# Optimization experiments

Measured on AMD Instinct MI355X. Metric: run time of the kernel, lower is better.

Reference implementation:

```python
import jax, jax.numpy as jnp
import numpy as np

N = 50000
E = 800000
IN_CH = 128
OUT_CH = 32
HEADS = 10
NEG_SLOPE = 0.2
NUM_GRAPHS = 512


def gat_layer(x, W, a_src, a_dst, b, src, dst, heads, out_ch):
    n = x.shape[0]
    h = (x @ W).reshape(n, heads, out_ch)            # [N,H,C]
    e_src = jnp.einsum('nhc,hc->nh', h, a_src)       # [N,H]
    e_dst = jnp.einsum('nhc,hc->nh', h, a_dst)       # [N,H]
    alpha = jax.nn.leaky_relu(e_src[src] + e_dst[dst], negative_slope=NEG_SLOPE)  # [E,H]
    amax = jax.ops.segment_max(alpha, dst, num_segments=n)
    amax = jnp.where(jnp.isneginf(amax), 0.0, amax)
    ex = jnp.exp(alpha - amax[dst])                   # [E,H]
    denom = jax.ops.segment_sum(ex, dst, num_segments=n)
    coef = ex / (denom[dst] + 1e-16)                  # segment softmax over incoming edges
    msg = h[src] * coef[:, :, None]                   # [E,H,C]
    out = jax.ops.segment_sum(msg, dst, num_segments=n)
    return out.reshape(n, heads * out_ch) + b


def setup_inputs() -> dict:
    key = jax.random.key(0)
    ks = jax.random.split(key, 12)
    x = jax.random.normal(ks[0], (N, IN_CH), dtype=jnp.float32)
    edge_index = jax.random.randint(ks[1], (2, E), 0, N, dtype=jnp.int32)
    batch = jnp.sort(jax.random.randint(ks[2], (N,), 0, NUM_GRAPHS, dtype=jnp.int32))
    s1 = 1.0 / np.sqrt(IN_CH)
    s2 = 1.0 / np.sqrt(HEADS * OUT_CH)
    s3 = 1.0 / np.sqrt(OUT_CH)
    W1 = jax.random.uniform(ks[3], (IN_CH, HEADS * OUT_CH), minval=-s1, maxval=s1, dtype=jnp.float32)
    a_src1 = jax.random.uniform(ks[4], (HEADS, OUT_CH), minval=-s3, maxval=s3, dtype=jnp.float32)
    a_dst1 = jax.random.uniform(ks[5], (HEADS, OUT_CH), minval=-s3, maxval=s3, dtype=jnp.float32)
    b1 = jnp.zeros((HEADS * OUT_CH,), dtype=jnp.float32)
    W2 = jax.random.uniform(ks[6], (HEADS * OUT_CH, OUT_CH), minval=-s2, maxval=s2, dtype=jnp.float32)
    a_src2 = jax.random.uniform(ks[7], (1, OUT_CH), minval=-s3, maxval=s3, dtype=jnp.float32)
    a_dst2 = jax.random.uniform(ks[8], (1, OUT_CH), minval=-s3, maxval=s3, dtype=jnp.float32)
    b2 = jnp.zeros((OUT_CH,), dtype=jnp.float32)
    fc_w = jax.random.uniform(ks[9], (OUT_CH, OUT_CH), minval=-s3, maxval=s3, dtype=jnp.float32)
    fc_b = jax.random.uniform(ks[10], (OUT_CH,), minval=-s3, maxval=s3, dtype=jnp.float32)
    return {
        'x': x, 'edge_index': edge_index, 'batch': batch, 'num_graphs': NUM_GRAPHS,
        'W1': W1, 'a_src1': a_src1, 'a_dst1': a_dst1, 'b1': b1,
        'W2': W2, 'a_src2': a_src2, 'a_dst2': a_dst2, 'b2': b2,
        'fc_w': fc_w, 'fc_b': fc_b,
    }


def reference(x, edge_index, batch, num_graphs, W1, a_src1, a_dst1, b1, W2, a_src2, a_dst2, b2, fc_w, fc_b):
    src, dst = edge_index[0], edge_index[1]
    h = gat_layer(x, W1, a_src1, a_dst1, b1, src, dst, HEADS, OUT_CH)
    h = jax.nn.elu(h)                                  # dropout = identity (eval)
    h = gat_layer(h, W2, a_src2, a_dst2, b2, src, dst, 1, OUT_CH)
    h = jax.nn.elu(h)
    pooled = jax.ops.segment_max(h, batch, num_segments=num_graphs)  # global max pool
    pooled = jnp.where(jnp.isneginf(pooled), 0.0, pooled)
    out = jax.nn.relu(pooled @ fc_w + fc_b)
    return out
```

## Files before the change

### kernel.cpp

```cpp
#include <hip/hip_runtime.h>

#define N_NODES 50000
#define N_EDGES 800000
#define IN_CH   128
#define OUT_CH  32
#define HEADS   10
#define HC      320
#define N_GRAPHS 512
#define NEG_SLOPE 0.2f
#define NBLK_SCAN 196

typedef __attribute__((ext_vector_type(8))) short bf16x8;
typedef __attribute__((ext_vector_type(4))) float f32x4;
typedef __attribute__((ext_vector_type(4))) unsigned short usx4;

__device__ __forceinline__ unsigned fmap(float f) {
  unsigned u = __float_as_uint(f);
  return (u & 0x80000000u) ? ~u : (u | 0x80000000u);
}
__device__ __forceinline__ float funmap(unsigned u) {
  u = (u & 0x80000000u) ? (u ^ 0x80000000u) : ~u;
  return __uint_as_float(u);
}
__device__ __forceinline__ float leaky(float a) {
  return a > 0.f ? a : NEG_SLOPE * a;
}
__device__ __forceinline__ unsigned short f2bf(float f) {
  unsigned u = __float_as_uint(f);
  return (unsigned short)((u + 0x7FFFu + ((u >> 16) & 1u)) >> 16);
}
__device__ __forceinline__ float bf2f(unsigned short b) {
  return __uint_as_float(((unsigned)b) << 16);
}
__device__ __forceinline__ float bflo(unsigned u) { return __uint_as_float(u << 16); }
__device__ __forceinline__ float bfhi(unsigned u) { return __uint_as_float(u & 0xFFFF0000u); }
__device__ __forceinline__ void store_split(unsigned short* __restrict__ ph,
                                            unsigned short* __restrict__ pl,
                                            size_t idx, float v) {
  unsigned short h = f2bf(v);
  ph[idx] = h;
  pl[idx] = f2bf(v - bf2f(h));
}
__device__ __forceinline__ float elu(float v) {
  return v > 0.f ? v : expm1f(v);
}

__global__ __launch_bounds__(256) void hist_k(const int* __restrict__ ei,
                                              int* __restrict__ deg) {
  int e = blockIdx.x * 256 + threadIdx.x;
  if (e < N_EDGES) atomicAdd(&deg[ei[N_EDGES + e]], 1);
}

__global__ __launch_bounds__(256) void scan_blk(const int* __restrict__ deg,
                                                int* __restrict__ roff,
                                                int* __restrict__ bsum) {
  __shared__ int s[256];
  int i = blockIdx.x * 256 + threadIdx.x;
  int v = (i < N_NODES) ? deg[i] : 0;
  s[threadIdx.x] = v;
  __syncthreads();
  #pragma unroll
  for (int o = 1; o < 256; o <<= 1) {
    int t = (threadIdx.x >= o) ? s[threadIdx.x - o] : 0;
    __syncthreads();
    s[threadIdx.x] += t;
    __syncthreads();
  }
  if (i < N_NODES) roff[i] = s[threadIdx.x] - v;
  if (threadIdx.x == 255) bsum[blockIdx.x] = s[255];
}

__global__ __launch_bounds__(256) void scan_top(int* __restrict__ bsum) {
  __shared__ int s[256];
  int i = threadIdx.x;
  int v = (i < NBLK_SCAN) ? bsum[i] : 0;
  s[i] = v;
  __syncthreads();
  #pragma unroll
  for (int o = 1; o < 256; o <<= 1) {
    int t = (i >= o) ? s[i - o] : 0;
    __syncthreads();
    s[i] += t;
    __syncthreads();
  }
  if (i < NBLK_SCAN) bsum[i] = s[i] - v;
}

__global__ __launch_bounds__(256) void scan_add(int* __restrict__ roff,
                                                const int* __restrict__ bsum) {
  int i = blockIdx.x * 256 + threadIdx.x;
  if (i < N_NODES) roff[i] += bsum[blockIdx.x];
  if (i == 0) roff[N_NODES] = N_EDGES;
}

__global__ __launch_bounds__(256) void scatter_k(const int* __restrict__ ei,
                                                 const int* __restrict__ roff,
                                                 int* __restrict__ cursor,
                                                 int* __restrict__ ssrc) {
  int e = blockIdx.x * 256 + threadIdx.x;
  if (e >= N_EDGES) return;
  int dst = ei[N_EDGES + e];
  int pos = roff[dst] + atomicAdd(&cursor[dst], 1);
  ssrc[pos] = ei[e];
}

__global__ __launch_bounds__(256) void conv_w(const float* __restrict__ W1,
                                              const float* __restrict__ W2,
                                              unsigned short* __restrict__ W1hT,
                                              unsigned short* __restrict__ W1lT,
                                              unsigned short* __restrict__ W2hT,
                                              unsigned short* __restrict__ W2lT) {
  int i = blockIdx.x * 256 + threadIdx.x;
  if (i < IN_CH * HC) {
    int n = i >> 7, k = i & 127;
    float v = W1[(size_t)k * HC + n];
    unsigned short h = f2bf(v);
    W1hT[i] = h; W1lT[i] = f2bf(v - bf2f(h));
  } else {
    int j = i - IN_CH * HC;
    if (j < OUT_CH * HC) {
      int c = j / HC, k = j - c * HC;
      float v = W2[(size_t)k * OUT_CH + c];
      unsigned short h = f2bf(v);
      W2hT[j] = h; W2lT[j] = f2bf(v - bf2f(h));
    }
  }
}

__global__ __launch_bounds__(256) void conv_wa(const float* __restrict__ W1,
                                               const float* __restrict__ a_src1,
                                               const float* __restrict__ a_dst1,
                                               unsigned short* __restrict__ W1hT,
                                               unsigned short* __restrict__ W1lT) {
  int i = blockIdx.x * 256 + threadIdx.x;
  if (i >= 32 * IN_CH) return;
  int j = i >> 7, k = i & 127;
  float v = 0.f;
  if (j < 20) {
    int head = (j < 10) ? j : (j - 10);
    const float* a = (j < 10) ? (a_src1 + head * OUT_CH) : (a_dst1 + head * OUT_CH);
    const float* wrow = W1 + (size_t)k * HC + head * OUT_CH;
    #pragma unroll
    for (int c = 0; c < OUT_CH; c++) v += wrow[c] * a[c];
  }
  unsigned short h = f2bf(v);
  W1hT[(size_t)(HC + j) * IN_CH + k] = h;
  W1lT[(size_t)(HC + j) * IN_CH + k] = f2bf(v - bf2f(h));
}

__global__ __launch_bounds__(256) void gemm1_mfma(const float* __restrict__ X,
                                                  const unsigned short* __restrict__ WhT,
                                                  const unsigned short* __restrict__ WlT,
                                                  unsigned short* __restrict__ Hb,
                                                  float* __restrict__ es,
                                                  float* __restrict__ ed) {
  const int wave = threadIdx.x >> 6;
  const int lane = threadIdx.x & 63;
  const int row0 = blockIdx.x * 64 + wave * 16;
  const int r = lane & 15;
  const int kg = lane >> 4;
  int arow = row0 + r; if (arow >= N_NODES) arow = N_NODES - 1;
  const float* xrow = X + (size_t)arow * IN_CH + kg * 8;
  const unsigned short* wb = WhT + (size_t)r * IN_CH + kg * 8;
  const unsigned short* lb = WlT + (size_t)r * IN_CH + kg * 8;
  f32x4 acc[22];
  #pragma unroll
  for (int c = 0; c < 22; c++) acc[c] = f32x4{0.f, 0.f, 0.f, 0.f};
  #pragma unroll
  for (int k0 = 0; k0 < IN_CH; k0 += 32) {
    float4 u = *reinterpret_cast<const float4*>(xrow + k0);
    float4 w = *reinterpret_cast<const float4*>(xrow + k0 + 4);
    float uv0 = u.x, uv1 = u.y, uv2 = u.z, uv3 = u.w;
    float uv4 = w.x, uv5 = w.y, uv6 = w.z, uv7 = w.w;
    bf16x8 ah, al;
    unsigned short hh;
    hh = f2bf(uv0); ah[0] = (short)hh; al[0] = (short)f2bf(uv0 - bf2f(hh));
    hh = f2bf(uv1); ah[1] = (short)hh; al[1] = (short)f2bf(uv1 - bf2f(hh));
    hh = f2bf(uv2); ah[2] = (short)hh; al[2] = (short)f2bf(uv2 - bf2f(hh));
    hh = f2bf(uv3); ah[3] = (short)hh; al[3] = (short)f2bf(uv3 - bf2f(hh));
    hh = f2bf(uv4); ah[4] = (short)hh; al[4] = (short)f2bf(uv4 - bf2f(hh));
    hh = f2bf(uv5); ah[5] = (short)hh; al[5] = (short)f2bf(uv5 - bf2f(hh));
    hh = f2bf(uv6); ah[6] = (short)hh; al[6] = (short)f2bf(uv6 - bf2f(hh));
    hh = f2bf(uv7); ah[7] = (short)hh; al[7] = (short)f2bf(uv7 - bf2f(hh));
    #pragma unroll
    for (int c = 0; c < 22; c++) {
      bf16x8 bh = *reinterpret_cast<const bf16x8*>(wb + (size_t)c * 16 * IN_CH + k0);
      bf16x8 bl = *reinterpret_cast<const bf16x8*>(lb + (size_t)c * 16 * IN_CH + k0);
      acc[c] = __builtin_amdgcn_mfma_f32_16x16x32_bf16(ah, bh, acc[c], 0, 0, 0);
      acc[c] = __builtin_amdgcn_mfma_f32_16x16x32_bf16(ah, bl, acc[c], 0, 0, 0);
      acc[c] = __builtin_amdgcn_mfma_f32_16x16x32_bf16(al, bh, acc[c], 0, 0, 0);
    }
  }
  const int crow0 = row0 + kg * 4;
  #pragma unroll
  for (int c = 0; c < 20; c++) {
    const int ccol = c * 16 + r;
    #pragma unroll
    for (int t = 0; t < 4; t++) {
      int rr = crow0 + t;
      if (rr < N_NODES) Hb[(size_t)rr * HC + ccol] = f2bf(acc[c][t]);
    }
  }
  #pragma unroll
  for (int t = 0; t < 4; t++) {
    int rr = crow0 + t;
    if (rr < N_NODES) {
      float v20 = acc[20][t];
      if (r < 10) es[rr * 10 + r] = v20;
      else        ed[rr * 10 + (r - 10)] = v20;
      if (r < 4)  ed[rr * 10 + 6 + r] = acc[21][t];
    }
  }
}

__global__ __launch_bounds__(256) void gemm2_mfma(const unsigned short* __restrict__ Ah,
                                                  const unsigned short* __restrict__ Al,
                                                  const unsigned short* __restrict__ WhT,
                                                  const unsigned short* __restrict__ WlT,
                                                  const float* __restrict__ a_src2,
                                                  const float* __restrict__ a_dst2,
                                                  float* __restrict__ H,
                                                  float* __restrict__ es,
                                                  float* __restrict__ ed) {
  const int wave = threadIdx.x >> 6;
  const int lane = threadIdx.x & 63;
  const int row0 = blockIdx.x * 64 + wave * 16;
  const int r = lane & 15;
  const int kg = lane >> 4;
  int arow = row0 + r; if (arow >= N_NODES) arow = N_NODES - 1;
  const unsigned short* ah_p = Ah + (size_t)arow * HC + kg * 8;
  const unsigned short* al_p = Al + (size_t)arow * HC + kg * 8;
  const unsigned short* wb = WhT + (size_t)r * HC + kg * 8;
  const unsigned short* lb = WlT + (size_t)r * HC + kg * 8;
  f32x4 acc[2];
  acc[0] = f32x4{0.f, 0.f, 0.f, 0.f};
  acc[1] = f32x4{0.f, 0.f, 0.f, 0.f};
  #pragma unroll
  for (int k0 = 0; k0 < HC; k0 += 32) {
    bf16x8 ah = *reinterpret_cast<const bf16x8*>(ah_p + k0);
    bf16x8 al = *reinterpret_cast<const bf16x8*>(al_p + k0);
    #pragma unroll
    for (int c = 0; c < 2; c++) {
      bf16x8 bh = *reinterpret_cast<const bf16x8*>(wb + (size_t)c * 16 * HC + k0);
      bf16x8 bl = *reinterpret_cast<const bf16x8*>(lb + (size_t)c * 16 * HC + k0);
      acc[c] = __builtin_amdgcn_mfma_f32_16x16x32_bf16(ah, bh, acc[c], 0, 0, 0);
      acc[c] = __builtin_amdgcn_mfma_f32_16x16x32_bf16(ah, bl, acc[c], 0, 0, 0);
      acc[c] = __builtin_amdgcn_mfma_f32_16x16x32_bf16(al, bh, acc[c], 0, 0, 0);
    }
  }
  const int crow0 = row0 + kg * 4;
  #pragma unroll
  for (int c = 0; c < 2; c++) {
    const int ccol = c * 16 + r;
    #pragma unroll
    for (int t = 0; t < 4; t++) {
      int rr = crow0 + t;
      if (rr < N_NODES) H[(size_t)rr * OUT_CH + ccol] = acc[c][t];
    }
  }
  const float as0 = a_src2[r], as1 = a_src2[16 + r];
  const float ad0 = a_dst2[r], ad1 = a_dst2[16 + r];
  float pe[4], pd[4];
  #pragma unroll
  for (int t = 0; t < 4; t++) {
    pe[t] = acc[0][t] * as0 + acc[1][t] * as1;
    pd[t] = acc[0][t] * ad0 + acc[1][t] * ad1;
  }
  #pragma unroll
  for (int o = 1; o < 16; o <<= 1) {
    #pragma unroll
    for (int t = 0; t < 4; t++) {
      pe[t] += __shfl_xor(pe[t], o);
      pd[t] += __shfl_xor(pd[t], o);
    }
  }
  if (r == 0) {
    #pragma unroll
    for (int t = 0; t < 4; t++) {
      int rr = crow0 + t;
      if (rr < N_NODES) { es[rr] = pe[t]; ed[rr] = pd[t]; }
    }
  }
}

__global__ __launch_bounds__(256) void agg1(const int* __restrict__ roff,
                                            const int* __restrict__ ssrc,
                                            const float* __restrict__ es,
                                            const float* __restrict__ ed,
                                            const unsigned short* __restrict__ h1b,
                                            const float* __restrict__ b1,
                                            unsigned short* __restrict__ acth,
                                            unsigned short* __restrict__ actl) {
  __shared__ float lds[4][64][11];
  const int n = (blockIdx.x * 256 + threadIdx.x) >> 6;
  if (n >= N_NODES) return;
  const int wslot = threadIdx.x >> 6;
  const int lane = threadIdx.x & 63;
  const int beg = roff[n];
  const int deg = roff[n + 1] - beg;

  if (deg == 0) {
    #pragma unroll
    for (int q = 0; q < 5; q++) {
      float v = elu(b1[lane + 64 * q]);
      store_split(acth, actl, (size_t)n * HC + lane + 64 * q, v);
    }
    return;
  }

  if (deg <= 64) {
    const int active = (lane < deg);
    const int src = ssrc[beg + (active ? lane : 0)];
    #pragma unroll
    for (int p = 0; p < 5; p++) {
      float2 edp = *reinterpret_cast<const float2*>(ed + n * 10 + 2 * p);
      float2 esp = *reinterpret_cast<const float2*>(es + src * 10 + 2 * p);
      lds[wslot][lane][2 * p]     = active ? expf(leaky(esp.x + edp.x)) : 0.f;
      lds[wslot][lane][2 * p + 1] = active ? expf(leaky(esp.y + edp.y)) : 0.f;
    }
    lds[wslot][lane][10] = __int_as_float(src * (HC * 2));

    const int half = lane >> 5;
    const int lc = lane & 31;
    const int hm = lc >> 2;
    const int ht = 8 + (lc >> 4);
    float accm[8] = {};
    float acct0 = 0.f, acct1 = 0.f, dm = 0.f, dt = 0.f;
    const int dege = (deg + 1) & ~1;
    const char* basem = reinterpret_cast<const char*>(h1b + 8 * lc);
    const char* baset = reinterpret_cast<const char*>(h1b + 256 + 2 * lc);
    for (int j = 0; j < dege; j += 2) {
      const int e = j + half;
      int off = __float_as_int(lds[wslot][e][10]);
      float cm = lds[wslot][e][hm];
      float ct = lds[wslot][e][ht];
      uint4 v = *reinterpret_cast<const uint4*>(basem + off);
      unsigned t = *reinterpret_cast<const unsigned*>(baset + off);
      unsigned w0 = v.x, w1 = v.y, w2 = v.z, w3 = v.w;
      accm[0] = fmaf(bflo(w0), cm, accm[0]);
      accm[1] = fmaf(bfhi(w0), cm, accm[1]);
      accm[2] = fmaf(bflo(w1), cm, accm[2]);
      accm[3] = fmaf(bfhi(w1), cm, accm[3]);
      accm[4] = fmaf(bflo(w2), cm, accm[4]);
      accm[5] = fmaf(bfhi(w2), cm, accm[5]);
      accm[6] = fmaf(bflo(w3), cm, accm[6]);
      accm[7] = fmaf(bfhi(w3), cm, accm[7]);
      acct0 = fmaf(bflo(t), ct, acct0);
      acct1 = fmaf(bfhi(t), ct, acct1);
      dm += cm;
      dt += ct;
    }
    #pragma unroll
    for (int k = 0; k < 8; k++) accm[k] += __shfl_xor(accm[k], 32);
    acct0 += __shfl_xor(acct0, 32);
    acct1 += __shfl_xor(acct1, 32);
    dm += __shfl_xor(dm, 32);
    dt += __shfl_xor(dt, 32);

    if (lane < 32) {
      const float invm = 1.f / (dm + 1e-16f);
      const size_t base = (size_t)n * HC;
      usx4 sh0, sl0, sh1, sl1;
      float vv;
      unsigned short hh;
      vv = elu(accm[0] * invm + b1[8 * lc + 0]); hh = f2bf(vv); sh0[0] = hh; sl0[0] = f2bf(vv - bf2f(hh));
      vv = elu(accm[1] * invm + b1[8 * lc + 1]); hh = f2bf(vv); sh0[1] = hh; sl0[1] = f2bf(vv - bf2f(hh));
      vv = elu(accm[2] * invm + b1[8 * lc + 2]); hh = f2bf(vv); sh0[2] = hh; sl0[2] = f2bf(vv - bf2f(hh));
      vv = elu(accm[3] * invm + b1[8 * lc + 3]); hh = f2bf(vv); sh0[3] = hh; sl0[3] = f2bf(vv - bf2f(hh));
      vv = elu(accm[4] * invm + b1[8 * lc + 4]); hh = f2bf(vv); sh1[0] = hh; sl1[0] = f2bf(vv - bf2f(hh));
      vv = elu(accm[5] * invm + b1[8 * lc + 5]); hh = f2bf(vv); sh1[1] = hh; sl1[1] = f2bf(vv - bf2f(hh));
      vv = elu(accm[6] * invm + b1[8 * lc + 6]); hh = f2bf(vv); sh1[2] = hh; sl1[2] = f2bf(vv - bf2f(hh));
      vv = elu(accm[7] * invm + b1[8 * lc + 7]); hh = f2bf(vv); sh1[3] = hh; sl1[3] = f2bf(vv - bf2f(hh));
      *reinterpret_cast<usx4*>(acth + base + 8 * lc) = sh0;
      *reinterpret_cast<usx4*>(acth + base + 8 * lc + 4) = sh1;
      *reinterpret_cast<usx4*>(actl + base + 8 * lc) = sl0;
      *reinterpret_cast<usx4*>(actl + base + 8 * lc + 4) = sl1;
      const float invt = 1.f / (dt + 1e-16f);
      unsigned tph, tpl;
      unsigned short h0, h1v, l0, l1v;
      vv = elu(acct0 * invt + b1[256 + 2 * lc + 0]); h0 = f2bf(vv); l0 = f2bf(vv - bf2f(h0));
      vv = elu(acct1 * invt + b1[256 + 2 * lc + 1]); h1v = f2bf(vv); l1v = f2bf(vv - bf2f(h1v));
      tph = (unsigned)h0 | ((unsigned)h1v << 16);
      tpl = (unsigned)l0 | ((unsigned)l1v << 16);
      *reinterpret_cast<unsigned*>(acth + base + 256 + 2 * lc) = tph;
      *reinterpret_cast<unsigned*>(actl + base + 256 + 2 * lc) = tpl;
    }
  } else {
    const int hb = lane >> 5;
    float acc[5] = {};
    float edv[5], m2[5];
    #pragma unroll
    for (int q = 0; q < 5; q++) { edv[q] = ed[n * 10 + 2 * q + hb]; m2[q] = -1e30f; }
    for (int j = beg; j < beg + deg; j++) {
      int src = ssrc[j];
      #pragma unroll
      for (int q = 0; q < 5; q++)
        m2[q] = fmaxf(m2[q], leaky(es[src * 10 + 2 * q + hb] + edv[q]));
    }
    float d2[5] = {};
    for (int j = beg; j < beg + deg; j++) {
      int src = ssrc[j];
      const unsigned short* hrow = h1b + (size_t)src * HC + lane;
      #pragma unroll
      for (int q = 0; q < 5; q++) {
        float ex = expf(leaky(es[src * 10 + 2 * q + hb] + edv[q]) - m2[q]);
        acc[q] = fmaf(bf2f(hrow[64 * q]), ex, acc[q]);
        d2[q] += ex;
      }
    }
    #pragma unroll
    for (int q = 0; q < 5; q++) {
      float v = elu(acc[q] / (d2[q] + 1e-16f) + b1[lane + 64 * q]);
      store_split(acth, actl, (size_t)n * HC + lane + 64 * q, v);
    }
  }
}

__global__ __launch_bounds__(256) void agg2(const int* __restrict__ roff,
                                            const int* __restrict__ ssrc,
                                            const float* __restrict__ es,
                                            const float* __restrict__ ed,
                                            const float* __restrict__ h2,
                                            const float* __restrict__ b2,
                                            const int* __restrict__ batch,
                                            unsigned* __restrict__ pooled) {
  __shared__ float lds[4][64][2];
  const int n = (blockIdx.x * 256 + threadIdx.x) >> 6;
  if (n >= N_NODES) return;
  const int wslot = threadIdx.x >> 6;
  const int lane = threadIdx.x & 63;
  const int c = lane & 31;
  const int hb = lane >> 5;
  const int beg = roff[n];
  const int deg = roff[n + 1] - beg;
  const int g = batch[n];

  if (deg == 0) {
    if (lane < 32) {
      float v = elu(b2[c]);
      atomicMax(&pooled[g * OUT_CH + c], fmap(v));
    }
    return;
  }

  float acc = 0.f, dacc = 0.f, dtot;

  if (deg <= 64) {
    const int active = (lane < deg);
    const int src = ssrc[beg + (active ? lane : 0)];
    const float edv = ed[n];
    float ex = active ? expf(leaky(es[src] + edv)) : 0.f;
    lds[wslot][lane][0] = ex;
    lds[wslot][lane][1] = __int_as_float(src * (OUT_CH * 4));
    const char* baseh = reinterpret_cast<const char*>(h2 + c);
    int j = hb;
    for (; j + 6 < deg; j += 8) {
      int o0 = __float_as_int(lds[wslot][j + 0][1]);
      int o1 = __float_as_int(lds[wslot][j + 2][1]);
      int o2 = __float_as_int(lds[wslot][j + 4][1]);
      int o3 = __float_as_int(lds[wslot][j + 6][1]);
      float c0 = lds[wslot][j + 0][0];
      float c1 = lds[wslot][j + 2][0];
      float c2 = lds[wslot][j + 4][0];
      float c3 = lds[wslot][j + 6][0];
      float v0 = *reinterpret_cast<const float*>(baseh + o0);
      float v1 = *reinterpret_cast<const float*>(baseh + o1);
      float v2 = *reinterpret_cast<const float*>(baseh + o2);
      float v3 = *reinterpret_cast<const float*>(baseh + o3);
      acc = fmaf(v0, c0, acc);
      acc = fmaf(v1, c1, acc);
      acc = fmaf(v2, c2, acc);
      acc = fmaf(v3, c3, acc);
      dacc += c0 + c1 + c2 + c3;
    }
    for (; j < deg; j += 2) {
      int oj = __float_as_int(lds[wslot][j][1]);
      float cj = lds[wslot][j][0];
      acc = fmaf(*reinterpret_cast<const float*>(baseh + oj), cj, acc);
      dacc += cj;
    }
    acc += __shfl_xor(acc, 32);
    dacc += __shfl_xor(dacc, 32);
    dtot = dacc;
  } else {
    const float edv = ed[n];
    float m = -1e30f;
    for (int j = beg; j < beg + deg; j++)
      m = fmaxf(m, leaky(es[ssrc[j]] + edv));
    float d = 0.f;
    for (int j = beg + hb; j < beg + deg; j += 2) {
      int src = ssrc[j];
      float ex = expf(leaky(es[src] + edv) - m);
      acc = fmaf(h2[(size_t)src * OUT_CH + c], ex, acc);
      d += ex;
    }
    acc += __shfl_xor(acc, 32);
    d += __shfl_xor(d, 32);
    dtot = d;
  }

  if (lane < 32) {
    float v = elu(acc / (dtot + 1e-16f) + b2[c]);
    atomicMax(&pooled[g * OUT_CH + c], fmap(v));
  }
}

__global__ __launch_bounds__(256) void final_k(const unsigned* __restrict__ pooled,
                                               const float* __restrict__ fc_w,
                                               const float* __restrict__ fc_b,
                                               float* __restrict__ out) {
  int idx = blockIdx.x * 256 + threadIdx.x;
  if (idx >= N_GRAPHS * OUT_CH) return;
  int g = idx >> 5, c = idx & 31;
  float s = fc_b[c];
  #pragma unroll
  for (int k = 0; k < OUT_CH; k++) {
    unsigned u = pooled[g * OUT_CH + k];
    float p = (u == 0u) ? 0.f : funmap(u);
    s += p * fc_w[k * OUT_CH + c];
  }
  out[idx] = s > 0.f ? s : 0.f;
}

extern "C" void kernel_launch(void* const* d_in, const int* in_sizes, int n_in,
                              void* d_out, int out_size, void* d_ws, size_t ws_size,
                              hipStream_t stream) {
  const float* x      = (const float*)d_in[0];
  const int*   ei     = (const int*)d_in[1];
  const int*   batch  = (const int*)d_in[2];
  const float* W1     = (const float*)d_in[4];
  const float* a_src1 = (const float*)d_in[5];
  const float* a_dst1 = (const float*)d_in[6];
  const float* b1     = (const float*)d_in[7];
  const float* W2     = (const float*)d_in[8];
  const float* a_src2 = (const float*)d_in[9];
  const float* a_dst2 = (const float*)d_in[10];
  const float* b2     = (const float*)d_in[11];
  const float* fc_w   = (const float*)d_in[12];
  const float* fc_b   = (const float*)d_in[13];
  float* out = (float*)d_out;

  char* ws = (char*)d_ws;
  unsigned short* h1b = (unsigned short*)(ws);
  float* h2   = (float*)(ws);
  unsigned short* acth = (unsigned short*)(ws + 64000000);
  unsigned short* actl = (unsigned short*)(ws + 96000000);
  char*  S    = ws + 128000000;
  int*   ssrc   = (int*)(S);
  int*   roff   = (int*)(S + 3200000);
  int*   deg    = (int*)(S + 3400064);
  int*   cursor = (int*)(S + 3600064);
  unsigned short* W1hT = (unsigned short*)(S + 3400064);
  unsigned short* W1lT = (unsigned short*)(S + 3400064 + 90112);
  unsigned short* W2hT = (unsigned short*)(S + 3400064 + 180224);
  unsigned short* W2lT = (unsigned short*)(S + 3400064 + 200704);
  float* es1    = (float*)(S + 3800064);
  float* ed1    = (float*)(S + 5800064);
  int*   bsum   = (int*)(S + 7800064);
  unsigned* pooled = (unsigned*)(S + 7801600);
  float* es2 = es1; float* ed2 = ed1;

  hipMemsetAsync(deg, 0, (size_t)N_NODES * 4, stream);
  hipMemsetAsync(cursor, 0, (size_t)N_NODES * 4, stream);
  hist_k   <<<(N_EDGES + 255) / 256, 256, 0, stream>>>(ei, deg);
  scan_blk <<<NBLK_SCAN, 256, 0, stream>>>(deg, roff, bsum);
  scan_top <<<1, 256, 0, stream>>>(bsum);
  scan_add <<<NBLK_SCAN, 256, 0, stream>>>(roff, bsum);
  scatter_k<<<(N_EDGES + 255) / 256, 256, 0, stream>>>(ei, roff, cursor, ssrc);

  conv_w<<<(IN_CH * HC + OUT_CH * HC + 255) / 256, 256, 0, stream>>>(
      W1, W2, W1hT, W1lT, W2hT, W2lT);
  conv_wa<<<(32 * IN_CH + 255) / 256, 256, 0, stream>>>(
      W1, a_src1, a_dst1, W1hT, W1lT);

  gemm1_mfma<<<(N_NODES + 63) / 64, 256, 0, stream>>>(x, W1hT, W1lT, h1b, es1, ed1);
  agg1 <<<(N_NODES * 64 + 255) / 256, 256, 0, stream>>>(roff, ssrc, es1, ed1, h1b, b1,
                                                        acth, actl);

  hipMemsetAsync(pooled, 0, (size_t)N_GRAPHS * OUT_CH * 4, stream);
  gemm2_mfma<<<(N_NODES + 63) / 64, 256, 0, stream>>>(acth, actl, W2hT, W2lT,
                                                      a_src2, a_dst2, h2, es2, ed2);
  agg2 <<<(N_NODES * 64 + 255) / 256, 256, 0, stream>>>(roff, ssrc, es2, ed2, h2, b2,
                                                        batch, pooled);
  final_k<<<(N_GRAPHS * OUT_CH + 255) / 256, 256, 0, stream>>>(pooled, fc_w, fc_b, out);
}
```

Measured before the change: 350.6 us.

## Sort nodes by degree and process two nodes per wavefront in aggregation

```diff
diff --git a/kernel.cpp b/kernel.cpp
--- a/kernel.cpp
+++ b/kernel.cpp
@@ -34,13 +34,6 @@
 }
 __device__ __forceinline__ float bflo(unsigned u) { return __uint_as_float(u << 16); }
 __device__ __forceinline__ float bfhi(unsigned u) { return __uint_as_float(u & 0xFFFF0000u); }
-__device__ __forceinline__ void store_split(unsigned short* __restrict__ ph,
-                                            unsigned short* __restrict__ pl,
-                                            size_t idx, float v) {
-  unsigned short h = f2bf(v);
-  ph[idx] = h;
-  pl[idx] = f2bf(v - bf2f(h));
-}
 __device__ __forceinline__ float elu(float v) {
   return v > 0.f ? v : expm1f(v);
 }
@@ -102,6 +95,40 @@
   int dst = ei[N_EDGES + e];
   int pos = roff[dst] + atomicAdd(&cursor[dst], 1);
   ssrc[pos] = ei[e];
+}
+
+__global__ __launch_bounds__(256) void dsort_hist(const int* __restrict__ roff,
+                                                  int* __restrict__ dh) {
+  int n = blockIdx.x * 256 + threadIdx.x;
+  if (n < N_NODES) {
+    int d = roff[n + 1] - roff[n];
+    atomicAdd(&dh[d > 255 ? 255 : d], 1);
+  }
+}
+__global__ __launch_bounds__(256) void dsort_scan(const int* __restrict__ dh,
+                                                  int* __restrict__ dcur) {
+  __shared__ int s[256];
+  int i = threadIdx.x;
+  int v = dh[i];
+  s[i] = v;
+  __syncthreads();
+  #pragma unroll
+  for (int o = 1; o < 256; o <<= 1) {
+    int t = (i >= o) ? s[i - o] : 0;
+    __syncthreads();
+    s[i] += t;
+    __syncthreads();
+  }
+  dcur[i] = s[i] - v;
+}
+__global__ __launch_bounds__(256) void dsort_scatter(const int* __restrict__ roff,
+                                                     int* __restrict__ dcur,
+                                                     int* __restrict__ nodeord) {
+  int n = blockIdx.x * 256 + threadIdx.x;
+  if (n >= N_NODES) return;
+  int d = roff[n + 1] - roff[n];
+  int pos = atomicAdd(&dcur[d > 255 ? 255 : d], 1);
+  nodeord[pos] = n;
 }
 
 __global__ __launch_bounds__(256) void conv_w(const float* __restrict__ W1,
@@ -289,53 +316,48 @@
                                             const float* __restrict__ ed,
                                             const unsigned short* __restrict__ h1b,
                                             const float* __restrict__ b1,
+                                            const int* __restrict__ nodeord,
                                             unsigned short* __restrict__ acth,
                                             unsigned short* __restrict__ actl) {
-  __shared__ float lds[4][64][11];
-  const int n = (blockIdx.x * 256 + threadIdx.x) >> 6;
-  if (n >= N_NODES) return;
+  __shared__ float lds[4][2][32][11];
+  const int wid = blockIdx.x * 4 + (threadIdx.x >> 6);
   const int wslot = threadIdx.x >> 6;
   const int lane = threadIdx.x & 63;
+  const int half = lane >> 5;
+  const int lc = lane & 31;
+  const int n = nodeord[2 * wid + half];
   const int beg = roff[n];
   const int deg = roff[n + 1] - beg;
-
-  if (deg == 0) {
-    #pragma unroll
-    for (int q = 0; q < 5; q++) {
-      float v = elu(b1[lane + 64 * q]);
-      store_split(acth, actl, (size_t)n * HC + lane + 64 * q, v);
-    }
-    return;
-  }
-
-  if (deg <= 64) {
-    const int active = (lane < deg);
-    const int src = ssrc[beg + (active ? lane : 0)];
+  const int degmax = max(deg, __shfl_xor(deg, 32));
+
+  const int hm = lc >> 2;
+  const int ht = 8 + (lc >> 4);
+  float accm[8] = {};
+  float acct0 = 0.f, acct1 = 0.f, dm = 0.f, dt = 0.f;
+  const char* basem = reinterpret_cast<const char*>(h1b + 8 * lc);
+  const char* baset = reinterpret_cast<const char*>(h1b + 256 + 2 * lc);
+
+  for (int t0 = 0; t0 < degmax; t0 += 32) {
+    const int e = t0 + lc;
+    const bool act = (e < deg);
+    const int src = act ? ssrc[beg + e] : 0;
     #pragma unroll
     for (int p = 0; p < 5; p++) {
       float2 edp = *reinterpret_cast<const float2*>(ed + n * 10 + 2 * p);
       float2 esp = *reinterpret_cast<const float2*>(es + src * 10 + 2 * p);
-      lds[wslot][lane][2 * p]     = active ? expf(leaky(esp.x + edp.x)) : 0.f;
-      lds[wslot][lane][2 * p + 1] = active ? expf(leaky(esp.y + edp.y)) : 0.f;
-    }
-    lds[wslot][lane][10] = __int_as_float(src * (HC * 2));
-
-    const int half = lane >> 5;
-    const int lc = lane & 31;
-    const int hm = lc >> 2;
-    const int ht = 8 + (lc >> 4);
-    float accm[8] = {};
-    float acct0 = 0.f, acct1 = 0.f, dm = 0.f, dt = 0.f;
-    const int dege = (deg + 1) & ~1;
-    const char* basem = reinterpret_cast<const char*>(h1b + 8 * lc);
-    const char* baset = reinterpret_cast<const char*>(h1b + 256 + 2 * lc);
-    for (int j = 0; j < dege; j += 2) {
-      const int e = j + half;
-      int off = __float_as_int(lds[wslot][e][10]);
-      float cm = lds[wslot][e][hm];
-      float ct = lds[wslot][e][ht];
+      lds[wslot][half][lc][2 * p]     = act ? expf(leaky(esp.x + edp.x)) : 0.f;
+      lds[wslot][half][lc][2 * p + 1] = act ? expf(leaky(esp.y + edp.y)) : 0.f;
+    }
+    lds[wslot][half][lc][10] = __int_as_float(src * (HC * 2));
+    int cnt = deg - t0;
+    cnt = cnt < 0 ? 0 : (cnt > 32 ? 32 : cnt);
+    const int cntm = max(cnt, __shfl_xor(cnt, 32));
+    for (int j = 0; j < cntm; j++) {
+      int off = __float_as_int(lds[wslot][half][j][10]);
+      float cm = lds[wslot][half][j][hm];
+      float ct = lds[wslot][half][j][ht];
       uint4 v = *reinterpret_cast<const uint4*>(basem + off);
-      unsigned t = *reinterpret_cast<const unsigned*>(baset + off);
+      unsigned tt = *reinterpret_cast<const unsigned*>(baset + off);
       unsigned w0 = v.x, w1 = v.y, w2 = v.z, w3 = v.w;
       accm[0] = fmaf(bflo(w0), cm, accm[0]);
       accm[1] = fmaf(bfhi(w0), cm, accm[1]);
@@ -345,75 +367,39 @@
       accm[5] = fmaf(bfhi(w2), cm, accm[5]);
       accm[6] = fmaf(bflo(w3), cm, accm[6]);
       accm[7] = fmaf(bfhi(w3), cm, accm[7]);
-      acct0 = fmaf(bflo(t), ct, acct0);
-      acct1 = fmaf(bfhi(t), ct, acct1);
+      acct0 = fmaf(bflo(tt), ct, acct0);
+      acct1 = fmaf(bfhi(tt), ct, acct1);
       dm += cm;
       dt += ct;
     }
-    #pragma unroll
-    for (int k = 0; k < 8; k++) accm[k] += __shfl_xor(accm[k], 32);
-    acct0 += __shfl_xor(acct0, 32);
-    acct1 += __shfl_xor(acct1, 32);
-    dm += __shfl_xor(dm, 32);
-    dt += __shfl_xor(dt, 32);
-
-    if (lane < 32) {
-      const float invm = 1.f / (dm + 1e-16f);
-      const size_t base = (size_t)n * HC;
-      usx4 sh0, sl0, sh1, sl1;
-      float vv;
-      unsigned short hh;
-      vv = elu(accm[0] * invm + b1[8 * lc + 0]); hh = f2bf(vv); sh0[0] = hh; sl0[0] = f2bf(vv - bf2f(hh));
-      vv = elu(accm[1] * invm + b1[8 * lc + 1]); hh = f2bf(vv); sh0[1] = hh; sl0[1] = f2bf(vv - bf2f(hh));
-      vv = elu(accm[2] * invm + b1[8 * lc + 2]); hh = f2bf(vv); sh0[2] = hh; sl0[2] = f2bf(vv - bf2f(hh));
-      vv = elu(accm[3] * invm + b1[8 * lc + 3]); hh = f2bf(vv); sh0[3] = hh; sl0[3] = f2bf(vv - bf2f(hh));
-      vv = elu(accm[4] * invm + b1[8 * lc + 4]); hh = f2bf(vv); sh1[0] = hh; sl1[0] = f2bf(vv - bf2f(hh));
-      vv = elu(accm[5] * invm + b1[8 * lc + 5]); hh = f2bf(vv); sh1[1] = hh; sl1[1] = f2bf(vv - bf2f(hh));
-      vv = elu(accm[6] * invm + b1[8 * lc + 6]); hh = f2bf(vv); sh1[2] = hh; sl1[2] = f2bf(vv - bf2f(hh));
-      vv = elu(accm[7] * invm + b1[8 * lc + 7]); hh = f2bf(vv); sh1[3] = hh; sl1[3] = f2bf(vv - bf2f(hh));
-      *reinterpret_cast<usx4*>(acth + base + 8 * lc) = sh0;
-      *reinterpret_cast<usx4*>(acth + base + 8 * lc + 4) = sh1;
-      *reinterpret_cast<usx4*>(actl + base + 8 * lc) = sl0;
-      *reinterpret_cast<usx4*>(actl + base + 8 * lc + 4) = sl1;
-      const float invt = 1.f / (dt + 1e-16f);
-      unsigned tph, tpl;
-      unsigned short h0, h1v, l0, l1v;
-      vv = elu(acct0 * invt + b1[256 + 2 * lc + 0]); h0 = f2bf(vv); l0 = f2bf(vv - bf2f(h0));
-      vv = elu(acct1 * invt + b1[256 + 2 * lc + 1]); h1v = f2bf(vv); l1v = f2bf(vv - bf2f(h1v));
-      tph = (unsigned)h0 | ((unsigned)h1v << 16);
-      tpl = (unsigned)l0 | ((unsigned)l1v << 16);
-      *reinterpret_cast<unsigned*>(acth + base + 256 + 2 * lc) = tph;
-      *reinterpret_cast<unsigned*>(actl + base + 256 + 2 * lc) = tpl;
-    }
-  } else {
-    const int hb = lane >> 5;
-    float acc[5] = {};
-    float edv[5], m2[5];
-    #pragma unroll
-    for (int q = 0; q < 5; q++) { edv[q] = ed[n * 10 + 2 * q + hb]; m2[q] = -1e30f; }
-    for (int j = beg; j < beg + deg; j++) {
-      int src = ssrc[j];
-      #pragma unroll
-      for (int q = 0; q < 5; q++)
-        m2[q] = fmaxf(m2[q], leaky(es[src * 10 + 2 * q + hb] + edv[q]));
-    }
-    float d2[5] = {};
-    for (int j = beg; j < beg + deg; j++) {
-      int src = ssrc[j];
-      const unsigned short* hrow = h1b + (size_t)src * HC + lane;
-      #pragma unroll
-      for (int q = 0; q < 5; q++) {
-        float ex = expf(leaky(es[src * 10 + 2 * q + hb] + edv[q]) - m2[q]);
-        acc[q] = fmaf(bf2f(hrow[64 * q]), ex, acc[q]);
-        d2[q] += ex;
-      }
-    }
-    #pragma unroll
-    for (int q = 0; q < 5; q++) {
-      float v = elu(acc[q] / (d2[q] + 1e-16f) + b1[lane + 64 * q]);
-      store_split(acth, actl, (size_t)n * HC + lane + 64 * q, v);
-    }
-  }
+  }
+
+  const float invm = 1.f / (dm + 1e-16f);
+  const float invt = 1.f / (dt + 1e-16f);
+  const size_t base = (size_t)n * HC;
+  usx4 sh0, sl0, sh1, sl1;
+  float vv;
+  unsigned short hh;
+  vv = elu(accm[0] * invm + b1[8 * lc + 0]); hh = f2bf(vv); sh0[0] = hh; sl0[0] = f2bf(vv - bf2f(hh));
+  vv = elu(accm[1] * invm + b1[8 * lc + 1]); hh = f2bf(vv); sh0[1] = hh; sl0[1] = f2bf(vv - bf2f(hh));
+  vv = elu(accm[2] * invm + b1[8 * lc + 2]); hh = f2bf(vv); sh0[2] = hh; sl0[2] = f2bf(vv - bf2f(hh));
+  vv = elu(accm[3] * invm + b1[8 * lc + 3]); hh = f2bf(vv); sh0[3] = hh; sl0[3] = f2bf(vv - bf2f(hh));
+  vv = elu(accm[4] * invm + b1[8 * lc + 4]); hh = f2bf(vv); sh1[0] = hh; sl1[0] = f2bf(vv - bf2f(hh));
+  vv = elu(accm[5] * invm + b1[8 * lc + 5]); hh = f2bf(vv); sh1[1] = hh; sl1[1] = f2bf(vv - bf2f(hh));
+  vv = elu(accm[6] * invm + b1[8 * lc + 6]); hh = f2bf(vv); sh1[2] = hh; sl1[2] = f2bf(vv - bf2f(hh));
+  vv = elu(accm[7] * invm + b1[8 * lc + 7]); hh = f2bf(vv); sh1[3] = hh; sl1[3] = f2bf(vv - bf2f(hh));
+  *reinterpret_cast<usx4*>(acth + base + 8 * lc) = sh0;
+  *reinterpret_cast<usx4*>(acth + base + 8 * lc + 4) = sh1;
+  *reinterpret_cast<usx4*>(actl + base + 8 * lc) = sl0;
+  *reinterpret_cast<usx4*>(actl + base + 8 * lc + 4) = sl1;
+  unsigned tph, tpl;
+  unsigned short h0, h1v, l0, l1v;
+  vv = elu(acct0 * invt + b1[256 + 2 * lc + 0]); h0 = f2bf(vv); l0 = f2bf(vv - bf2f(h0));
+  vv = elu(acct1 * invt + b1[256 + 2 * lc + 1]); h1v = f2bf(vv); l1v = f2bf(vv - bf2f(h1v));
+  tph = (unsigned)h0 | ((unsigned)h1v << 16);
+  tpl = (unsigned)l0 | ((unsigned)l1v << 16);
+  *reinterpret_cast<unsigned*>(acth + base + 256 + 2 * lc) = tph;
+  *reinterpret_cast<unsigned*>(actl + base + 256 + 2 * lc) = tpl;
 }
 
 __global__ __launch_bounds__(256) void agg2(const int* __restrict__ roff,
@@ -423,86 +409,41 @@
                                             const float* __restrict__ h2,
                                             const float* __restrict__ b2,
                                             const int* __restrict__ batch,
+                                            const int* __restrict__ nodeord,
                                             unsigned* __restrict__ pooled) {
-  __shared__ float lds[4][64][2];
-  const int n = (blockIdx.x * 256 + threadIdx.x) >> 6;
-  if (n >= N_NODES) return;
+  __shared__ float lds[4][2][32][2];
+  const int wid = blockIdx.x * 4 + (threadIdx.x >> 6);
   const int wslot = threadIdx.x >> 6;
   const int lane = threadIdx.x & 63;
-  const int c = lane & 31;
-  const int hb = lane >> 5;
+  const int half = lane >> 5;
+  const int lc = lane & 31;
+  const int n = nodeord[2 * wid + half];
   const int beg = roff[n];
   const int deg = roff[n + 1] - beg;
-  const int g = batch[n];
-
-  if (deg == 0) {
-    if (lane < 32) {
-      float v = elu(b2[c]);
-      atomicMax(&pooled[g * OUT_CH + c], fmap(v));
-    }
-    return;
-  }
-
-  float acc = 0.f, dacc = 0.f, dtot;
-
-  if (deg <= 64) {
-    const int active = (lane < deg);
-    const int src = ssrc[beg + (active ? lane : 0)];
-    const float edv = ed[n];
-    float ex = active ? expf(leaky(es[src] + edv)) : 0.f;
-    lds[wslot][lane][0] = ex;
-    lds[wslot][lane][1] = __int_as_float(src * (OUT_CH * 4));
-    const char* baseh = reinterpret_cast<const char*>(h2 + c);
-    int j = hb;
-    for (; j + 6 < deg; j += 8) {
-      int o0 = __float_as_int(lds[wslot][j + 0][1]);
-      int o1 = __float_as_int(lds[wslot][j + 2][1]);
-      int o2 = __float_as_int(lds[wslot][j + 4][1]);
-      int o3 = __float_as_int(lds[wslot][j + 6][1]);
-      float c0 = lds[wslot][j + 0][0];
-      float c1 = lds[wslot][j + 2][0];
-      float c2 = lds[wslot][j + 4][0];
-      float c3 = lds[wslot][j + 6][0];
-      float v0 = *reinterpret_cast<const float*>(baseh + o0);
-      float v1 = *reinterpret_cast<const float*>(baseh + o1);
-      float v2 = *reinterpret_cast<const float*>(baseh + o2);
-      float v3 = *reinterpret_cast<const float*>(baseh + o3);
-      acc = fmaf(v0, c0, acc);
-      acc = fmaf(v1, c1, acc);
-      acc = fmaf(v2, c2, acc);
-      acc = fmaf(v3, c3, acc);
-      dacc += c0 + c1 + c2 + c3;
-    }
-    for (; j < deg; j += 2) {
-      int oj = __float_as_int(lds[wslot][j][1]);
-      float cj = lds[wslot][j][0];
-      acc = fmaf(*reinterpret_cast<const float*>(baseh + oj), cj, acc);
+  const int degmax = max(deg, __shfl_xor(deg, 32));
+  const float edv = ed[n];
+
+  float acc = 0.f, dacc = 0.f;
+  const char* baseh = reinterpret_cast<const char*>(h2 + lc);
+
+  for (int t0 = 0; t0 < degmax; t0 += 32) {
+    const int e = t0 + lc;
+    const bool act = (e < deg);
+    const int src = act ? ssrc[beg + e] : 0;
+    lds[wslot][half][lc][0] = act ? expf(leaky(es[src] + edv)) : 0.f;
+    lds[wslot][half][lc][1] = __int_as_float(src * (OUT_CH * 4));
+    int cnt = deg - t0;
+    cnt = cnt < 0 ? 0 : (cnt > 32 ? 32 : cnt);
+    const int cntm = max(cnt, __shfl_xor(cnt, 32));
+    for (int j = 0; j < cntm; j++) {
+      int off = __float_as_int(lds[wslot][half][j][1]);
+      float cj = lds[wslot][half][j][0];
+      acc = fmaf(*reinterpret_cast<const float*>(baseh + off), cj, acc);
       dacc += cj;
     }
-    acc += __shfl_xor(acc, 32);
-    dacc += __shfl_xor(dacc, 32);
-    dtot = dacc;
-  } else {
-    const float edv = ed[n];
-    float m = -1e30f;
-    for (int j = beg; j < beg + deg; j++)
-      m = fmaxf(m, leaky(es[ssrc[j]] + edv));
-    float d = 0.f;
-    for (int j = beg + hb; j < beg + deg; j += 2) {
-      int src = ssrc[j];
-      float ex = expf(leaky(es[src] + edv) - m);
-      acc = fmaf(h2[(size_t)src * OUT_CH + c], ex, acc);
-      d += ex;
-    }
-    acc += __shfl_xor(acc, 32);
-    d += __shfl_xor(d, 32);
-    dtot = d;
-  }
-
-  if (lane < 32) {
-    float v = elu(acc / (dtot + 1e-16f) + b2[c]);
-    atomicMax(&pooled[g * OUT_CH + c], fmap(v));
-  }
+  }
+  float v = elu(acc / (dacc + 1e-16f) + b2[lc]);
+  atomicMax(&pooled[batch[n] * OUT_CH + lc], fmap(v));
 }
 
 __global__ __launch_bounds__(256) void final_k(const unsigned* __restrict__ pooled,
@@ -543,6 +484,9 @@
   char* ws = (char*)d_ws;
   unsigned short* h1b = (unsigned short*)(ws);
   float* h2   = (float*)(ws);
+  int*   nodeord = (int*)(ws + 40000000);
+  int*   dh      = (int*)(ws + 40200064);
+  int*   dcur    = (int*)(ws + 40201088);
   unsigned short* acth = (unsigned short*)(ws + 64000000);
   unsigned short* actl = (unsigned short*)(ws + 96000000);
   char*  S    = ws + 128000000;
@@ -568,19 +512,24 @@
   scan_add <<<NBLK_SCAN, 256, 0, stream>>>(roff, bsum);
   scatter_k<<<(N_EDGES + 255) / 256, 256, 0, stream>>>(ei, roff, cursor, ssrc);
 
+  hipMemsetAsync(dh, 0, 1024, stream);
+  dsort_hist   <<<NBLK_SCAN, 256, 0, stream>>>(roff, dh);
+  dsort_scan   <<<1, 256, 0, stream>>>(dh, dcur);
+  dsort_scatter<<<NBLK_SCAN, 256, 0, stream>>>(roff, dcur, nodeord);
+
   conv_w<<<(IN_CH * HC + OUT_CH * HC + 255) / 256, 256, 0, stream>>>(
       W1, W2, W1hT, W1lT, W2hT, W2lT);
   conv_wa<<<(32 * IN_CH + 255) / 256, 256, 0, stream>>>(
       W1, a_src1, a_dst1, W1hT, W1lT);
 
   gemm1_mfma<<<(N_NODES + 63) / 64, 256, 0, stream>>>(x, W1hT, W1lT, h1b, es1, ed1);
-  agg1 <<<(N_NODES * 64 + 255) / 256, 256, 0, stream>>>(roff, ssrc, es1, ed1, h1b, b1,
-                                                        acth, actl);
+  agg1 <<<N_NODES / 8, 256, 0, stream>>>(roff, ssrc, es1, ed1, h1b, b1, nodeord,
+                                         acth, actl);
 
   hipMemsetAsync(pooled, 0, (size_t)N_GRAPHS * OUT_CH * 4, stream);
   gemm2_mfma<<<(N_NODES + 63) / 64, 256, 0, stream>>>(acth, actl, W2hT, W2lT,
                                                       a_src2, a_dst2, h2, es2, ed2);
-  agg2 <<<(N_NODES * 64 + 255) / 256, 256, 0, stream>>>(roff, ssrc, es2, ed2, h2, b2,
-                                                        batch, pooled);
+  agg2 <<<N_NODES / 8, 256, 0, stream>>>(roff, ssrc, es2, ed2, h2, b2, batch, nodeord,
+                                         pooled);
   final_k<<<(N_GRAPHS * OUT_CH + 255) / 256, 256, 0, stream>>>(pooled, fc_w, fc_b, out);
 }
```

Result: slower. 618.2 us (+76.3%).
